# Kernel optimization log

Hardware: AMD Instinct MI355X
Metric: run time of the kernel (lower is better)

Reference implementation:

```python
import jax, jax.numpy as jnp
import numpy as np

N_NODES = 50000
N_GRAPHS = 16
NEG_SLOPE = 0.2


def gat_layer(x, W, a_s, a_d, b, src, dst, num_nodes):
    # h: [N, out]
    h = x @ W
    # per-node attention logits (heads=1)
    al_s = (h * a_s).sum(-1)  # [N]
    al_d = (h * a_d).sum(-1)  # [N]
    e = jax.nn.leaky_relu(al_s[src] + al_d[dst], NEG_SLOPE)  # [E]
    # segment softmax over incoming edges of each destination node
    m = jax.ops.segment_max(e, dst, num_segments=num_nodes)
    p = jnp.exp(e - m[dst])
    z = jax.ops.segment_sum(p, dst, num_segments=num_nodes)
    coef = p / z[dst]  # self-loops guarantee z > 0
    out = jax.ops.segment_sum(coef[:, None] * h[src], dst, num_segments=num_nodes)
    return out + b


def setup_inputs() -> dict:
    key = jax.random.key(0)
    ks = jax.random.split(key, 20)
    in_dim, hid, out_dim = 256, 128, 128
    E = 800000
    x = jax.random.normal(ks[0], (N_NODES, in_dim), dtype=jnp.float32)
    edge_index = jax.random.randint(ks[1], (2, E), 0, N_NODES, dtype=jnp.int32)
    batch = jnp.sort(jax.random.randint(ks[2], (N_NODES,), 0, N_GRAPHS, dtype=jnp.int32))

    def glorot(k, shape):
        fan = shape[0] + shape[-1]
        s = jnp.sqrt(6.0 / fan)
        return jax.random.uniform(k, shape, jnp.float32, -s, s)

    dims = [(in_dim, hid), (hid, hid), (hid, out_dim)]
    inp = {"x": x, "edge_index": edge_index, "batch": batch}
    for i, (di, do) in enumerate(dims):
        inp[f"W{i}"] = glorot(ks[3 + 4 * i], (di, do))
        inp[f"as{i}"] = glorot(ks[4 + 4 * i], (1, do))[0]
        inp[f"ad{i}"] = glorot(ks[5 + 4 * i], (1, do))[0]
        inp[f"b{i}"] = jnp.zeros((do,), jnp.float32)
    return inp


def reference(x, edge_index, batch, W0, as0, ad0, b0, W1, as1, ad1, b1, W2, as2, ad2, b2):
    # add self loops once (PyG GATConv add_self_loops=True)
    loops = jnp.arange(N_NODES, dtype=edge_index.dtype)
    src = jnp.concatenate([edge_index[0], loops])
    dst = jnp.concatenate([edge_index[1], loops])

    h = gat_layer(x, W0, as0, ad0, b0, src, dst, N_NODES)
    h = jax.nn.relu(h)  # act; dropout is identity at eval
    h = gat_layer(h, W1, as1, ad1, b1, src, dst, N_NODES)
    h = jax.nn.relu(h)
    node_emb = gat_layer(h, W2, as2, ad2, b2, src, dst, N_NODES)

    # global_mean_pool
    b32 = batch.astype(jnp.int32)
    sums = jax.ops.segment_sum(node_emb, b32, num_segments=N_GRAPHS)
    cnt = jax.ops.segment_sum(jnp.ones((N_NODES,), node_emb.dtype), b32, num_segments=N_GRAPHS)
    return sums / jnp.maximum(cnt, 1.0)[:, None]
```

## Files before the change

kernel.cpp:

```cpp
#include <hip/hip_runtime.h>
#include <math.h>

#define NN 50000
#define NE 800000
#define NTE (NE + NN)
#define NG 16
#define HID 128
#define NEG_SLOPE 0.2f

#define NBUK 391
#define SLOT 2560
#define EPW 4096
#define NWG_E ((NTE + EPW - 1) / EPW)
#define GEMM_GRID ((NN + 63) / 64)

#define AS_PAD 136
#define SMEM_BYTES 52224

typedef __attribute__((ext_vector_type(8))) __bf16 bf16x8;
typedef __attribute__((ext_vector_type(4))) float f32x4;

union V16 {
    float4 f4;
    uint4 u4;
    bf16x8 b8;
    __bf16 h[8];
};

__global__ void k_prep(int* __restrict__ bwr, float* __restrict__ sums,
                       int* __restrict__ off,
                       const float* __restrict__ W0, const float* __restrict__ W1,
                       const float* __restrict__ W2, __bf16* __restrict__ Wt0,
                       __bf16* __restrict__ Wt1, __bf16* __restrict__ Wt2) {
    int t = blockIdx.x * blockDim.x + threadIdx.x;
    if (t == 0) off[NN] = NTE;
    if (t <= NBUK) bwr[t] = 0;
    if (t < NG * HID) sums[t] = 0.0f;
    if (t < 256 * HID) {
        int k = t >> 7, n = t & 127;
        Wt0[(size_t)n * 256 + k] = (__bf16)W0[t];
    } else if (t < 256 * HID + HID * HID) {
        int u = t - 256 * HID;
        int k = u >> 7, n = u & 127;
        Wt1[(size_t)n * HID + k] = (__bf16)W1[u];
    } else if (t < 256 * HID + 2 * HID * HID) {
        int u = t - 256 * HID - HID * HID;
        int k = u >> 7, n = u & 127;
        Wt2[(size_t)n * HID + k] = (__bf16)W2[u];
    }
}

__device__ __forceinline__ void scatter_body(const int* __restrict__ ei,
                                             int* __restrict__ bwr,
                                             int* __restrict__ rec, int blk,
                                             char* smem) {
    int* hist = (int*)smem;
    int* cur = hist + NBUK;
    int t = threadIdx.x;
    for (int b = t; b < NBUK; b += 256) hist[b] = 0;
    __syncthreads();
    int base = blk * EPW;
    #pragma unroll
    for (int r = 0; r < EPW / 256; r++) {
        int idx = base + r * 256 + t;
        if (idx < NTE) {
            int dst = (idx < NE) ? ei[NE + idx] : (idx - NE);
            atomicAdd(&hist[dst >> 7], 1);
        }
    }
    __syncthreads();
    for (int b = t; b < NBUK; b += 256) {
        int c = hist[b];
        if (c) cur[b] = atomicAdd(&bwr[b], c);
    }
    __syncthreads();
    #pragma unroll
    for (int r = 0; r < EPW / 256; r++) {
        int idx = base + r * 256 + t;
        if (idx < NTE) {
            int src, dst;
            if (idx < NE) { src = ei[idx]; dst = ei[NE + idx]; }
            else          { src = idx - NE; dst = src; }
            int b = dst >> 7;
            int pos = atomicAdd(&cur[b], 1);
            rec[(size_t)b * SLOT + pos] = src | ((dst & 127) << 17);
        }
    }
}

__device__ __forceinline__ void scan512(const int* __restrict__ bwr, int* s) {
    int t = threadIdx.x;
    s[t] = (t < NBUK) ? bwr[t] : 0;
    s[t + 256] = (t + 256 < NBUK) ? bwr[t + 256] : 0;
    __syncthreads();
    for (int o = 1; o < 512; o <<= 1) {
        int a0 = (t >= o) ? s[t - o] : 0;
        int a1 = s[t + 256 - o];
        __syncthreads();
        s[t] += a0;
        s[t + 256] += a1;
        __syncthreads();
    }
}

__global__ __launch_bounds__(256) void k_bfill(const int* __restrict__ bwr,
                                               const int* __restrict__ rec,
                                               int* __restrict__ off,
                                               int* __restrict__ csr) {
    __shared__ int s[512];
    __shared__ int cnt[128];
    __shared__ int scn[128];
    __shared__ int cur[128];
    int b = blockIdx.x, t = threadIdx.x;
    scan512(bwr, s);
    int base = s[b] - bwr[b];
    int n = bwr[b];
    const int* rb = rec + (size_t)b * SLOT;
    if (t < 128) cnt[t] = 0;
    __syncthreads();
    for (int i = t; i < n; i += 256) atomicAdd(&cnt[rb[i] >> 17], 1);
    __syncthreads();
    if (t < 128) scn[t] = cnt[t];
    __syncthreads();
    #pragma unroll
    for (int o = 1; o < 128; o <<= 1) {
        int add = (t >= o && t < 128) ? scn[t - o] : 0;
        __syncthreads();
        if (t < 128) scn[t] += add;
        __syncthreads();
    }
    if (t < 128) {
        int ex = scn[t] - cnt[t];
        cur[t] = ex;
        int d = b * 128 + t;
        if (d < NN) off[d] = base + ex;
    }
    __syncthreads();
    for (int i = t; i < n; i += 256) {
        int r = rb[i];
        int dloc = r >> 17;
        int src = r & 131071;
        int pos = atomicAdd(&cur[dloc], 1);
        csr[base + pos] = src;
    }
}

template <typename AT>
__device__ __forceinline__ void gemm_body(const AT* __restrict__ A,
                                          const __bf16* __restrict__ Bt,
                                          __bf16* __restrict__ C,
                                          const float* __restrict__ a_s,
                                          const float* __restrict__ a_d,
                                          float* __restrict__ als,
                                          float* __restrict__ ald,
                                          int M, int K, int blk, char* smem) {
    __bf16(*As)[AS_PAD] = (__bf16(*)[AS_PAD])smem;
    __bf16(*Bs)[AS_PAD] = (__bf16(*)[AS_PAD])(smem + 17408);

    int tid = threadIdx.x;
    int rowBase = blk * 64;
    int wv = tid >> 6;
    int lane = tid & 63;
    int g = lane >> 4;
    int c = lane & 15;

    f32x4 acc[8];
    #pragma unroll
    for (int ni = 0; ni < 8; ni++) acc[ni] = (f32x4){0.f, 0.f, 0.f, 0.f};

    for (int k0 = 0; k0 < K; k0 += 128) {
        if (k0) __syncthreads();
        #pragma unroll
        for (int rep = 0; rep < 4; rep++) {
            int ch = rep * 256 + tid;
            int r = ch >> 4, q = ch & 15;
            int row = rowBase + r;
            if constexpr (sizeof(AT) == 2) {
                float4 v = {0.f, 0.f, 0.f, 0.f};
                if (row < M) v = *(const float4*)((const __bf16*)A + (size_t)row * K + k0 + q * 8);
                *(float4*)&As[r][q * 8] = v;
            } else {
                float vv[8] = {0.f, 0.f, 0.f, 0.f, 0.f, 0.f, 0.f, 0.f};
                if (row < M) {
                    const float* Ap = (const float*)A + (size_t)row * K + k0 + q * 8;
                    float4 v0 = *(const float4*)Ap;
                    float4 v1 = *(const float4*)(Ap + 4);
                    vv[0] = v0.x; vv[1] = v0.y; vv[2] = v0.z; vv[3] = v0.w;
                    vv[4] = v1.x; vv[5] = v1.y; vv[6] = v1.z; vv[7] = v1.w;
                }
                V16 o;
                #pragma unroll
                for (int t = 0; t < 8; t++) o.h[t] = (__bf16)vv[t];
                *(float4*)&As[r][q * 8] = o.f4;
            }
        }
        #pragma unroll
        for (int rep = 0; rep < 8; rep++) {
            int ch = rep * 256 + tid;
            int r = ch >> 4, q = ch & 15;
            float4 v = *(const float4*)(Bt + (size_t)r * K + k0 + q * 8);
            *(float4*)&Bs[r][q * 8] = v;
        }
        __syncthreads();

        #pragma unroll
        for (int kc = 0; kc < 4; kc++) {
            bf16x8 a = *(const bf16x8*)&As[wv * 16 + c][kc * 32 + g * 8];
            #pragma unroll
            for (int ni = 0; ni < 8; ni++) {
                bf16x8 b = *(const bf16x8*)&Bs[ni * 16 + c][kc * 32 + g * 8];
                acc[ni] = __builtin_amdgcn_mfma_f32_16x16x32_bf16(a, b, acc[ni], 0, 0, 0);
            }
        }
    }

    float asv[8], adv[8];
    #pragma unroll
    for (int ni = 0; ni < 8; ni++) {
        asv[ni] = a_s[ni * 16 + c];
        adv[ni] = a_d[ni * 16 + c];
    }
    int rb = rowBase + wv * 16 + g * 4;
    #pragma unroll
    for (int i = 0; i < 4; i++) {
        int row = rb + i;
        float s = 0.f, dd = 0.f;
        #pragma unroll
        for (int ni = 0; ni < 8; ni++) {
            float v = acc[ni][i];
            s = fmaf(v, asv[ni], s);
            dd = fmaf(v, adv[ni], dd);
        }
        #pragma unroll
        for (int o = 1; o <= 8; o <<= 1) {
            s += __shfl_xor(s, o);
            dd += __shfl_xor(dd, o);
        }
        if (row < M) {
            #pragma unroll
            for (int ni = 0; ni < 8; ni++)
                C[(size_t)row * HID + ni * 16 + c] = (__bf16)acc[ni][i];
            if (c == 0) {
                als[row] = s;
                ald[row] = dd;
            }
        }
    }
}

__global__ __launch_bounds__(256) void k_gemm_bf16(const __bf16* __restrict__ A,
                                                   const __bf16* __restrict__ Bt,
                                                   __bf16* __restrict__ C,
                                                   const float* __restrict__ a_s,
                                                   const float* __restrict__ a_d,
                                                   float* __restrict__ als,
                                                   float* __restrict__ ald) {
    __shared__ __align__(16) char smem[SMEM_BYTES];
    gemm_body<__bf16>(A, Bt, C, a_s, a_d, als, ald, NN, HID, blockIdx.x, smem);
}

__global__ __launch_bounds__(256) void k_gemm0_scatter(const float* __restrict__ x,
                                                       const __bf16* __restrict__ Wt0,
                                                       __bf16* __restrict__ C,
                                                       const float* __restrict__ a_s,
                                                       const float* __restrict__ a_d,
                                                       float* __restrict__ als,
                                                       float* __restrict__ ald,
                                                       const int* __restrict__ ei,
                                                       int* __restrict__ bwr,
                                                       int* __restrict__ rec) {
    __shared__ __align__(16) char smem[SMEM_BYTES];
    if (blockIdx.x < GEMM_GRID) {
        gemm_body<float>(x, Wt0, C, a_s, a_d, als, ald, NN, 256, blockIdx.x, smem);
    } else {
        scatter_body(ei, bwr, rec, blockIdx.x - GEMM_GRID, smem);
    }
}

__global__ __launch_bounds__(256) void k_attn(const __bf16* __restrict__ h,
                                              const float* __restrict__ als,
                                              const float* __restrict__ ald,
                                              const int* __restrict__ off,
                                              const int* __restrict__ csr,
                                              const float* __restrict__ bias,
                                              __bf16* __restrict__ yout,
                                              int do_relu) {
    __shared__ int2 s_e[4][64];
    int gt = blockIdx.x * blockDim.x + threadIdx.x;
    int d = gt >> 6;
    int lane = gt & 63;
    if (d >= NN) return;
    int wv = threadIdx.x >> 6;
    int grp = lane >> 4;
    int c = lane & 15;

    int e0 = off[d], e1 = off[d + 1];
    int deg = e1 - e0;
    float ald_d = ald[d];
    float acc[8] = {0.f, 0.f, 0.f, 0.f, 0.f, 0.f, 0.f, 0.f};

    if (deg <= 64) {
        int s = 0;
        float e = -INFINITY;
        if (lane < deg) {
            s = csr[e0 + lane];
            float t = als[s] + ald_d;
            e = (t > 0.0f) ? t : NEG_SLOPE * t;
        }
        float mx = e;
        #pragma unroll
        for (int o = 32; o > 0; o >>= 1) mx = fmaxf(mx, __shfl_xor(mx, o));
        float p = (lane < deg) ? __expf(e - mx) : 0.0f;
        float z = p;
        #pragma unroll
        for (int o = 32; o > 0; o >>= 1) z += __shfl_xor(z, o);
        float inv_z = 1.0f / z;
        s_e[wv][lane] = make_int2(s, __float_as_int(p * inv_z));

        int degR = (deg + 3) & ~3;
        #pragma unroll 4
        for (int k = grp; k < degR; k += 4) {
            int2 pr = s_e[wv][k];
            int ss = pr.x;
            float cf = __int_as_float(pr.y);
            V16 v;
            v.f4 = *(const float4*)(h + (size_t)ss * HID + c * 8);
            #pragma unroll
            for (int i = 0; i < 4; i++) {
                unsigned int u = (&v.u4.x)[i];
                float lo = __uint_as_float(u << 16);
                float hi = __uint_as_float(u & 0xffff0000u);
                acc[2 * i]     = fmaf(cf, lo, acc[2 * i]);
                acc[2 * i + 1] = fmaf(cf, hi, acc[2 * i + 1]);
            }
        }
    } else {
        float mx = -INFINITY;
        for (int j = e0 + lane; j < e1; j += 64) {
            float t = als[csr[j]] + ald_d;
            t = (t > 0.0f) ? t : NEG_SLOPE * t;
            mx = fmaxf(mx, t);
        }
        #pragma unroll
        for (int o = 32; o > 0; o >>= 1) mx = fmaxf(mx, __shfl_xor(mx, o));
        float z = 0.0f;
        for (int j = e0 + lane; j < e1; j += 64) {
            float t = als[csr[j]] + ald_d;
            t = (t > 0.0f) ? t : NEG_SLOPE * t;
            z += __expf(t - mx);
        }
        #pragma unroll
        for (int o = 32; o > 0; o >>= 1) z += __shfl_xor(z, o);
        float inv_z = 1.0f / z;
        for (int k = grp; k < deg; k += 4) {
            int ss = csr[e0 + k];
            float t = als[ss] + ald_d;
            t = (t > 0.0f) ? t : NEG_SLOPE * t;
            float cf = __expf(t - mx) * inv_z;
            V16 v;
            v.f4 = *(const float4*)(h + (size_t)ss * HID + c * 8);
            #pragma unroll
            for (int i = 0; i < 4; i++) {
                unsigned int u = (&v.u4.x)[i];
                float lo = __uint_as_float(u << 16);
                float hi = __uint_as_float(u & 0xffff0000u);
                acc[2 * i]     = fmaf(cf, lo, acc[2 * i]);
                acc[2 * i + 1] = fmaf(cf, hi, acc[2 * i + 1]);
            }
        }
    }

    #pragma unroll
    for (int t = 0; t < 8; t++) {
        acc[t] += __shfl_xor(acc[t], 16);
        acc[t] += __shfl_xor(acc[t], 32);
    }

    if (grp == 0) {
        float4 b0 = *(const float4*)(bias + c * 8);
        float4 b1 = *(const float4*)(bias + c * 8 + 4);
        acc[0] += b0.x; acc[1] += b0.y; acc[2] += b0.z; acc[3] += b0.w;
        acc[4] += b1.x; acc[5] += b1.y; acc[6] += b1.z; acc[7] += b1.w;
        if (do_relu) {
            #pragma unroll
            for (int t = 0; t < 8; t++) acc[t] = fmaxf(acc[t], 0.0f);
        }
        V16 o;
        #pragma unroll
        for (int t = 0; t < 8; t++) o.h[t] = (__bf16)acc[t];
        *(float4*)(yout + (size_t)d * HID + c * 8) = o.f4;
    }
}

__global__ void k_pool(const __bf16* __restrict__ emb, const int* __restrict__ batch,
                       float* __restrict__ sums) {
    int t = threadIdx.x;
    int base = blockIdx.x * 64;
    int end = base + 64;
    if (end > NN) end = NN;
    float acc = 0.0f;
    int g_cur = -1;
    for (int n = base; n < end; ++n) {
        int g = batch[n];
        if (g != g_cur) {
            if (g_cur >= 0) atomicAdd(&sums[g_cur * HID + t], acc);
            acc = 0.0f;
            g_cur = g;
        }
        acc += (float)emb[(size_t)n * HID + t];
    }
    if (g_cur >= 0) atomicAdd(&sums[g_cur * HID + t], acc);
}

__global__ void k_div(const float* __restrict__ sums, const int* __restrict__ batch,
                      float* __restrict__ out) {
    int i = blockIdx.x * blockDim.x + threadIdx.x;
    if (i >= NG * HID) return;
    int g = i >> 7;
    int lo = 0, hi = NN;
    while (lo < hi) { int mid = (lo + hi) >> 1; if (batch[mid] < g) lo = mid + 1; else hi = mid; }
    int lo2 = lo, hi2 = NN;
    while (lo2 < hi2) { int mid = (lo2 + hi2) >> 1; if (batch[mid] < g + 1) lo2 = mid + 1; else hi2 = mid; }
    int c = lo2 - lo;
    out[i] = sums[i] / (float)(c > 1 ? c : 1);
}

extern "C" void kernel_launch(void* const* d_in, const int* in_sizes, int n_in,
                              void* d_out, int out_size, void* d_ws, size_t ws_size,
                              hipStream_t stream) {
    const float* x     = (const float*)d_in[0];
    const int*   ei    = (const int*)d_in[1];
    const int*   batch = (const int*)d_in[2];
    const float* W[3]  = {(const float*)d_in[3], (const float*)d_in[7], (const float*)d_in[11]};
    const float* AS[3] = {(const float*)d_in[4], (const float*)d_in[8], (const float*)d_in[12]};
    const float* AD[3] = {(const float*)d_in[5], (const float*)d_in[9], (const float*)d_in[13]};
    const float* BI[3] = {(const float*)d_in[6], (const float*)d_in[10], (const float*)d_in[14]};
    float* out = (float*)d_out;

    char* ws = (char*)d_ws;
    size_t o = 0;
    auto alloc = [&](size_t bytes) {
        void* p = ws + o;
        o = (o + bytes + 255) & ~(size_t)255;
        return p;
    };
    __bf16* hb  = (__bf16*)alloc((size_t)NN * HID * 2);
    __bf16* yb  = (__bf16*)alloc((size_t)NN * HID * 2);
    __bf16* Wt0 = (__bf16*)alloc((size_t)256 * HID * 2);
    __bf16* Wt1 = (__bf16*)alloc((size_t)HID * HID * 2);
    __bf16* Wt2 = (__bf16*)alloc((size_t)HID * HID * 2);
    float* als  = (float*)alloc(NN * 4);
    float* ald  = (float*)alloc(NN * 4);
    int* off    = (int*)alloc((NN + 1) * 4);
    int* bwr    = (int*)alloc((NBUK + 1) * 4);
    int* rec    = (int*)alloc((size_t)NBUK * SLOT * 4);
    int* csr    = (int*)alloc((size_t)NTE * 4);
    float* sums = (float*)alloc(NG * HID * 4);
    (void)ws_size; (void)in_sizes; (void)n_in; (void)out_size;

    const int wave_grid = (NN * 64 + 255) / 256;

    k_prep<<<(256 * HID + 2 * HID * HID + 255) / 256, 256, 0, stream>>>(
        bwr, sums, off, W[0], W[1], W[2], Wt0, Wt1, Wt2);

    k_gemm0_scatter<<<GEMM_GRID + NWG_E, 256, 0, stream>>>(
        x, Wt0, hb, AS[0], AD[0], als, ald, ei, bwr, rec);

    k_bfill<<<NBUK, 256, 0, stream>>>(bwr, rec, off, csr);

    k_attn<<<wave_grid, 256, 0, stream>>>(hb, als, ald, off, csr, BI[0], yb, 1);

    k_gemm_bf16<<<GEMM_GRID, 256, 0, stream>>>(yb, Wt1, hb, AS[1], AD[1], als, ald);
    k_attn<<<wave_grid, 256, 0, stream>>>(hb, als, ald, off, csr, BI[1], yb, 1);

    k_gemm_bf16<<<GEMM_GRID, 256, 0, stream>>>(yb, Wt2, hb, AS[2], AD[2], als, ald);
    k_attn<<<wave_grid, 256, 0, stream>>>(hb, als, ald, off, csr, BI[2], yb, 0);

    k_pool<<<(NN + 63) / 64, 128, 0, stream>>>(yb, batch, sums);
    k_div<<<(NG * HID + 255) / 256, 256, 0, stream>>>(sums, batch, out);
}
```

Before: 307.5 us.

## Drop LDS staging in GEMM, load MFMA operands directly from global memory

Result: slower. 339.4 us (+10.4%).

```diff
diff --git a/kernel.cpp b/kernel.cpp
--- a/kernel.cpp
+++ b/kernel.cpp
@@ -13,9 +13,6 @@
 #define EPW 4096
 #define NWG_E ((NTE + EPW - 1) / EPW)
 #define GEMM_GRID ((NN + 63) / 64)
-
-#define AS_PAD 136
-#define SMEM_BYTES 52224
 
 typedef __attribute__((ext_vector_type(8))) __bf16 bf16x8;
 typedef __attribute__((ext_vector_type(4))) float f32x4;
@@ -52,10 +49,9 @@
 
 __device__ __forceinline__ void scatter_body(const int* __restrict__ ei,
                                              int* __restrict__ bwr,
-                                             int* __restrict__ rec, int blk,
-                                             char* smem) {
-    int* hist = (int*)smem;
-    int* cur = hist + NBUK;
+                                             int* __restrict__ rec, int blk) {
+    __shared__ int hist[NBUK];
+    __shared__ int cur[NBUK];
     int t = threadIdx.x;
     for (int b = t; b < NBUK; b += 256) hist[b] = 0;
     __syncthreads();
@@ -145,7 +141,7 @@
     }
 }
 
-template <typename AT>
+template <typename AT, int K>
 __device__ __forceinline__ void gemm_body(const AT* __restrict__ A,
                                           const __bf16* __restrict__ Bt,
                                           __bf16* __restrict__ C,
@@ -153,10 +149,7 @@
                                           const float* __restrict__ a_d,
                                           float* __restrict__ als,
                                           float* __restrict__ ald,
-                                          int M, int K, int blk, char* smem) {
-    __bf16(*As)[AS_PAD] = (__bf16(*)[AS_PAD])smem;
-    __bf16(*Bs)[AS_PAD] = (__bf16(*)[AS_PAD])(smem + 17408);
-
+                                          int M, int blk) {
     int tid = threadIdx.x;
     int rowBase = blk * 64;
     int wv = tid >> 6;
@@ -164,53 +157,39 @@
     int g = lane >> 4;
     int c = lane & 15;
 
+    int rowA = rowBase + wv * 16 + c;
+    bool va = rowA < M;
+
     f32x4 acc[8];
     #pragma unroll
     for (int ni = 0; ni < 8; ni++) acc[ni] = (f32x4){0.f, 0.f, 0.f, 0.f};
 
-    for (int k0 = 0; k0 < K; k0 += 128) {
-        if (k0) __syncthreads();
-        #pragma unroll
-        for (int rep = 0; rep < 4; rep++) {
-            int ch = rep * 256 + tid;
-            int r = ch >> 4, q = ch & 15;
-            int row = rowBase + r;
-            if constexpr (sizeof(AT) == 2) {
-                float4 v = {0.f, 0.f, 0.f, 0.f};
-                if (row < M) v = *(const float4*)((const __bf16*)A + (size_t)row * K + k0 + q * 8);
-                *(float4*)&As[r][q * 8] = v;
-            } else {
-                float vv[8] = {0.f, 0.f, 0.f, 0.f, 0.f, 0.f, 0.f, 0.f};
-                if (row < M) {
-                    const float* Ap = (const float*)A + (size_t)row * K + k0 + q * 8;
-                    float4 v0 = *(const float4*)Ap;
-                    float4 v1 = *(const float4*)(Ap + 4);
-                    vv[0] = v0.x; vv[1] = v0.y; vv[2] = v0.z; vv[3] = v0.w;
-                    vv[4] = v1.x; vv[5] = v1.y; vv[6] = v1.z; vv[7] = v1.w;
-                }
-                V16 o;
-                #pragma unroll
-                for (int t = 0; t < 8; t++) o.h[t] = (__bf16)vv[t];
-                *(float4*)&As[r][q * 8] = o.f4;
+    #pragma unroll
+    for (int kc = 0; kc < K / 32; kc++) {
+        bf16x8 a;
+        if constexpr (sizeof(AT) == 2) {
+            V16 t;
+            t.f4 = (float4){0.f, 0.f, 0.f, 0.f};
+            if (va) t.f4 = *(const float4*)((const __bf16*)A + (size_t)rowA * K + kc * 32 + g * 8);
+            a = t.b8;
+        } else {
+            float vv[8] = {0.f, 0.f, 0.f, 0.f, 0.f, 0.f, 0.f, 0.f};
+            if (va) {
+                const float* Ap = (const float*)A + (size_t)rowA * K + kc * 32 + g * 8;
+                float4 v0 = *(const float4*)Ap;
+                float4 v1 = *(const float4*)(Ap + 4);
+                vv[0] = v0.x; vv[1] = v0.y; vv[2] = v0.z; vv[3] = v0.w;
+                vv[4] = v1.x; vv[5] = v1.y; vv[6] = v1.z; vv[7] = v1.w;
             }
-        }
-        #pragma unroll
-        for (int rep = 0; rep < 8; rep++) {
-            int ch = rep * 256 + tid;
-            int r = ch >> 4, q = ch & 15;
-            float4 v = *(const float4*)(Bt + (size_t)r * K + k0 + q * 8);
-            *(float4*)&Bs[r][q * 8] = v;
-        }
-        __syncthreads();
-
-        #pragma unroll
-        for (int kc = 0; kc < 4; kc++) {
-            bf16x8 a = *(const bf16x8*)&As[wv * 16 + c][kc * 32 + g * 8];
+            V16 t;
             #pragma unroll
-            for (int ni = 0; ni < 8; ni++) {
-                bf16x8 b = *(const bf16x8*)&Bs[ni * 16 + c][kc * 32 + g * 8];
-                acc[ni] = __builtin_amdgcn_mfma_f32_16x16x32_bf16(a, b, acc[ni], 0, 0, 0);
-            }
+            for (int q = 0; q < 8; q++) t.h[q] = (__bf16)vv[q];
+            a = t.b8;
+        }
+        #pragma unroll
+        for (int ni = 0; ni < 8; ni++) {
+            bf16x8 b = *(const bf16x8*)(Bt + (size_t)(ni * 16 + c) * K + kc * 32 + g * 8);
+            acc[ni] = __builtin_amdgcn_mfma_f32_16x16x32_bf16(a, b, acc[ni], 0, 0, 0);
         }
     }
 
@@ -255,8 +234,7 @@
                                                    const float* __restrict__ a_d,
                                                    float* __restrict__ als,
                                                    float* __restrict__ ald) {
-    __shared__ __align__(16) char smem[SMEM_BYTES];
-    gemm_body<__bf16>(A, Bt, C, a_s, a_d, als, ald, NN, HID, blockIdx.x, smem);
+    gemm_body<__bf16, HID>(A, Bt, C, a_s, a_d, als, ald, NN, blockIdx.x);
 }
 
 __global__ __launch_bounds__(256) void k_gemm0_scatter(const float* __restrict__ x,
@@ -269,11 +247,10 @@
                                                        const int* __restrict__ ei,
                                                        int* __restrict__ bwr,
                                                        int* __restrict__ rec) {
-    __shared__ __align__(16) char smem[SMEM_BYTES];
     if (blockIdx.x < GEMM_GRID) {
-        gemm_body<float>(x, Wt0, C, a_s, a_d, als, ald, NN, 256, blockIdx.x, smem);
+        gemm_body<float, 256>(x, Wt0, C, a_s, a_d, als, ald, NN, blockIdx.x);
     } else {
-        scatter_body(ei, bwr, rec, blockIdx.x - GEMM_GRID, smem);
+        scatter_body(ei, bwr, rec, blockIdx.x - GEMM_GRID);
     }
 }
 
```
